# Kernel optimization log

Measured on AMD Instinct MI355X. Metric: run time of the kernel, lower is better.

Reference implementation:

```python
import jax, jax.numpy as jnp
import numpy as np

POLY_DEGREE = 3
LOW, MID, HIGH = 3, 6, 9
K = LOW + MID + HIGH  # 18 total harmonics
NUM_POINTS = 128 ** 3
BATCH = 4


def _band_sum(t, a, b, omega):
    """sum_k a_k*cos(w_k t) + b_k*sin(w_k t) without materializing [B,N,K].
    t: [B,N]; a,b: [N,k]; omega: [k]. Scans over the small harmonic axis."""
    def step(acc, xs):
        a_k, b_k, w = xs  # a_k,b_k: [N], w: scalar
        ph = w * t  # [B,N]
        return acc + a_k[None, :] * jnp.cos(ph) + b_k[None, :] * jnp.sin(ph), None
    acc0 = jnp.zeros_like(t)
    acc, _ = jax.lax.scan(step, acc0, (a.T, b.T, omega))
    return acc


def setup_inputs() -> dict:
    key = jax.random.key(0)
    k1, k2, k3, k4 = jax.random.split(key, 4)
    input_t = jax.random.uniform(k1, (BATCH,), dtype=jnp.float32)  # times in [0,1)
    poly_coeffs = jax.random.normal(k2, (NUM_POINTS, POLY_DEGREE + 1), dtype=jnp.float32) * 0.1
    fourier_a = jax.random.normal(k3, (NUM_POINTS, K), dtype=jnp.float32) * 0.1
    fourier_b = jax.random.normal(k4, (NUM_POINTS, K), dtype=jnp.float32) * 0.1
    return {
        "input_t": input_t,
        "poly_coeffs": poly_coeffs,
        "fourier_a": fourier_a,
        "fourier_b": fourier_b,
        "model_stage": 3,
    }


def reference(input_t, poly_coeffs, fourier_a, fourier_b, model_stage):
    B = input_t.shape[0]
    N = poly_coeffs.shape[0]
    t = jnp.broadcast_to(input_t[:, None], (B, N))  # [B, N]
    curr_stage = min(model_stage, 3) if model_stage >= 0 else 3
    omega = 2.0 * jnp.pi * jnp.arange(1, K + 1, dtype=jnp.float32)

    y_poly = jnp.zeros((B, N), dtype=jnp.float32)
    if POLY_DEGREE > 0 and curr_stage >= 0:
        for i in range(POLY_DEGREE + 1):
            y_poly = y_poly + poly_coeffs[:, i][None, :] * t ** i

    y_fourier = jnp.zeros((B, N), dtype=jnp.float32)
    bands = [(0, LOW, 1), (LOW, LOW + MID, 2), (LOW + MID, K, 3)]
    for s, e, req_stage in bands:
        if e > s and curr_stage >= req_stage:
            y_fourier = y_fourier + _band_sum(
                t, fourier_a[:, s:e], fourier_b[:, s:e], omega[s:e]
            )
    return y_poly, y_fourier
```

## Files before the change

kernel.cpp:

```cpp
#include <hip/hip_runtime.h>

#define KH 18
#define NPTS (128*128*128)
#define BB 4

__global__ __launch_bounds__(256) void dddm_kernel(
    const float* __restrict__ input_t,
    const float* __restrict__ poly,
    const float* __restrict__ fa,
    const float* __restrict__ fb,
    const int*   __restrict__ stage_p,
    float* __restrict__ out)
{
    __shared__ float ct[BB][KH];
    __shared__ float st[BB][KH];
    __shared__ float tp[BB][4];

    const int tid = threadIdx.x;
    if (tid < BB * KH) {
        const int b = tid / KH, k = tid % KH;
        const float t = input_t[b];
        const float ph = 6.283185307179586f * (float)(k + 1) * t;
        float s, c;
        sincosf(ph, &s, &c);
        ct[b][k] = c;
        st[b][k] = s;
    } else if (tid < BB * KH + BB) {
        const int b = tid - BB * KH;
        const float t = input_t[b];
        tp[b][0] = 1.0f;
        tp[b][1] = t;
        tp[b][2] = t * t;
        tp[b][3] = t * t * t;
    }

    const int ms = *stage_p;
    const int cs = (ms >= 0) ? (ms < 3 ? ms : 3) : 3;
    const int kmax = (cs >= 3) ? 18 : (cs == 2 ? 9 : (cs == 1 ? 3 : 0));

    __syncthreads();

    const int n = blockIdx.x * blockDim.x + threadIdx.x;
    if (n >= NPTS) return;

    const float4 c4 = reinterpret_cast<const float4*>(poly)[n];
    float yp[BB];
#pragma unroll
    for (int b = 0; b < BB; ++b)
        yp[b] = c4.x * tp[b][0] + c4.y * tp[b][1] + c4.z * tp[b][2] + c4.w * tp[b][3];

    float yf[BB] = {0.f, 0.f, 0.f, 0.f};
    if (kmax == KH) {
        float2 a2[9], b2[9];
        const float2* ar = reinterpret_cast<const float2*>(fa + (size_t)n * KH);
        const float2* br = reinterpret_cast<const float2*>(fb + (size_t)n * KH);
#pragma unroll
        for (int j = 0; j < 9; ++j) { a2[j] = ar[j]; b2[j] = br[j]; }
        const float* av = reinterpret_cast<const float*>(a2);
        const float* bv = reinterpret_cast<const float*>(b2);
#pragma unroll
        for (int k = 0; k < KH; ++k) {
            const float ak = av[k], bk = bv[k];
#pragma unroll
            for (int b = 0; b < BB; ++b)
                yf[b] += ak * ct[b][k] + bk * st[b][k];
        }
    } else if (kmax > 0) {
        for (int k = 0; k < kmax; ++k) {
            const float ak = fa[(size_t)n * KH + k];
            const float bk = fb[(size_t)n * KH + k];
#pragma unroll
            for (int b = 0; b < BB; ++b)
                yf[b] += ak * ct[b][k] + bk * st[b][k];
        }
    }

#pragma unroll
    for (int b = 0; b < BB; ++b) {
        out[(size_t)b * NPTS + n]            = yp[b];
        out[(size_t)(BB + b) * NPTS + n]     = yf[b];
    }
}

extern "C" void kernel_launch(void* const* d_in, const int* in_sizes, int n_in,
                              void* d_out, int out_size, void* d_ws, size_t ws_size,
                              hipStream_t stream) {
    const float* input_t = (const float*)d_in[0];
    const float* poly    = (const float*)d_in[1];
    const float* fa      = (const float*)d_in[2];
    const float* fb      = (const float*)d_in[3];
    const int*   stage   = (const int*)d_in[4];
    float* out = (float*)d_out;

    dddm_kernel<<<NPTS / 256, 256, 0, stream>>>(input_t, poly, fa, fb, stage, out);
}
```

Before: 351.1 us.

## Stage Fourier coefficient rows through shared memory with coalesced float4 loads

Each block now loads its contiguous chunk of fourier_a and fourier_b rows with fully coalesced float4 loads into a 36 KB shared-memory buffer. Each thread then reads its own 18-float rows from LDS instead of issuing strided float2 global loads. It also sets a minimum-blocks hint in launch bounds. The aim is better global-memory coalescing on a bandwidth-bound kernel, at the cost of LDS capacity, which may limit occupancy, and possible LDS bank conflicts from the stride-18 reads.

Result: no change. 349.3 us (-0.5%).

```diff
diff --git a/kernel.cpp b/kernel.cpp
--- a/kernel.cpp
+++ b/kernel.cpp
@@ -3,8 +3,10 @@
 #define KH 18
 #define NPTS (128*128*128)
 #define BB 4
+#define BLK 256
+#define ROW_FLOATS (BLK * KH)
 
-__global__ __launch_bounds__(256) void dddm_kernel(
+__global__ __launch_bounds__(256, 4) void dddm_kernel(
     const float* __restrict__ input_t,
     const float* __restrict__ poly,
     const float* __restrict__ fa,
@@ -12,19 +14,22 @@
     const int*   __restrict__ stage_p,
     float* __restrict__ out)
 {
+    __shared__ float s[2 * ROW_FLOATS];
     __shared__ float ct[BB][KH];
     __shared__ float st[BB][KH];
     __shared__ float tp[BB][4];
 
     const int tid = threadIdx.x;
+    const int n0  = blockIdx.x * BLK;
+
     if (tid < BB * KH) {
         const int b = tid / KH, k = tid % KH;
         const float t = input_t[b];
         const float ph = 6.283185307179586f * (float)(k + 1) * t;
-        float s, c;
-        sincosf(ph, &s, &c);
-        ct[b][k] = c;
-        st[b][k] = s;
+        float sn, cs;
+        sincosf(ph, &sn, &cs);
+        ct[b][k] = cs;
+        st[b][k] = sn;
     } else if (tid < BB * KH + BB) {
         const int b = tid - BB * KH;
         const float t = input_t[b];
@@ -34,14 +39,29 @@
         tp[b][3] = t * t * t;
     }
 
+    const float4* fa4 = reinterpret_cast<const float4*>(fa + (size_t)n0 * KH);
+    const float4* fb4 = reinterpret_cast<const float4*>(fb + (size_t)n0 * KH);
+    float4* s4 = reinterpret_cast<float4*>(s);
+
+    float4 v[9];
+#pragma unroll
+    for (int j = 0; j < 9; ++j) {
+        const int idx = j * BLK + tid;
+        v[j] = (idx < ROW_FLOATS / 4) ? fa4[idx] : fb4[idx - ROW_FLOATS / 4];
+    }
+#pragma unroll
+    for (int j = 0; j < 9; ++j) {
+        const int idx = j * BLK + tid;
+        s4[idx] = v[j];
+    }
+
     const int ms = *stage_p;
     const int cs = (ms >= 0) ? (ms < 3 ? ms : 3) : 3;
     const int kmax = (cs >= 3) ? 18 : (cs == 2 ? 9 : (cs == 1 ? 3 : 0));
 
     __syncthreads();
 
-    const int n = blockIdx.x * blockDim.x + threadIdx.x;
-    if (n >= NPTS) return;
+    const int n = n0 + tid;
 
     const float4 c4 = reinterpret_cast<const float4*>(poly)[n];
     float yp[BB];
@@ -49,15 +69,21 @@
     for (int b = 0; b < BB; ++b)
         yp[b] = c4.x * tp[b][0] + c4.y * tp[b][1] + c4.z * tp[b][2] + c4.w * tp[b][3];
 
+    float av[KH], bv[KH];
+    {
+        const float2* ar = reinterpret_cast<const float2*>(s + tid * KH);
+        const float2* br = reinterpret_cast<const float2*>(s + ROW_FLOATS + tid * KH);
+#pragma unroll
+        for (int j = 0; j < 9; ++j) {
+            const float2 a2 = ar[j];
+            const float2 b2 = br[j];
+            av[2 * j] = a2.x; av[2 * j + 1] = a2.y;
+            bv[2 * j] = b2.x; bv[2 * j + 1] = b2.y;
+        }
+    }
+
     float yf[BB] = {0.f, 0.f, 0.f, 0.f};
     if (kmax == KH) {
-        float2 a2[9], b2[9];
-        const float2* ar = reinterpret_cast<const float2*>(fa + (size_t)n * KH);
-        const float2* br = reinterpret_cast<const float2*>(fb + (size_t)n * KH);
-#pragma unroll
-        for (int j = 0; j < 9; ++j) { a2[j] = ar[j]; b2[j] = br[j]; }
-        const float* av = reinterpret_cast<const float*>(a2);
-        const float* bv = reinterpret_cast<const float*>(b2);
 #pragma unroll
         for (int k = 0; k < KH; ++k) {
             const float ak = av[k], bk = bv[k];
@@ -67,8 +93,7 @@
         }
     } else if (kmax > 0) {
         for (int k = 0; k < kmax; ++k) {
-            const float ak = fa[(size_t)n * KH + k];
-            const float bk = fb[(size_t)n * KH + k];
+            const float ak = av[k], bk = bv[k];
 #pragma unroll
             for (int b = 0; b < BB; ++b)
                 yf[b] += ak * ct[b][k] + bk * st[b][k];
@@ -77,8 +102,8 @@
 
 #pragma unroll
     for (int b = 0; b < BB; ++b) {
-        out[(size_t)b * NPTS + n]            = yp[b];
-        out[(size_t)(BB + b) * NPTS + n]     = yf[b];
+        out[(size_t)b * NPTS + n]        = yp[b];
+        out[(size_t)(BB + b) * NPTS + n] = yf[b];
     }
 }
 
@@ -92,5 +117,5 @@
     const int*   stage   = (const int*)d_in[4];
     float* out = (float*)d_out;
 
-    dddm_kernel<<<NPTS / 256, 256, 0, stream>>>(input_t, poly, fa, fb, stage, out);
+    dddm_kernel<<<NPTS / BLK, BLK, 0, stream>>>(input_t, poly, fa, fb, stage, out);
 }
```
